# Kernel tuning notes

Measured on AMD Instinct MI355X. Metric: run time of the kernel, lower is better.

## Reference

```python
import jax, jax.numpy as jnp
import numpy as np

SR = 48000
TIME_LENGTH = 62400  # int(1.3 * 48000)
MAX_VOICES = 16


def _conv1d_same(x, k, b):
    # x: [B, L, Cin], k: [K, Cin, Cout] -> [B, L, Cout], keras Conv1D padding='same'
    y = jax.lax.conv_general_dilated(x, k, (1,), 'SAME', dimension_numbers=('NWC', 'WIO', 'NWC'))
    return y + b


def setup_inputs() -> dict:
    key = jax.random.key(0)
    ks = jax.random.split(key, 20)
    B, L, D, C = 16, 250, 128, 32
    V = MAX_VOICES
    din = D + C
    w = lambda k, s: jax.random.normal(k, s, jnp.float32) * 0.05
    inp = {}
    inp['base_signal'] = jax.random.normal(ks[0], (B, TIME_LENGTH), jnp.float32)
    inp['z'] = jax.random.normal(ks[1], (B, L, D), jnp.float32)
    inp['cond'] = jax.random.uniform(ks[2], (B, C), jnp.float32)
    inp['fundamental_freq'] = jax.random.uniform(ks[3], (B,), jnp.float32)
    # param_predictor: Dense(256)->Dense(128)->Dense(64)->Dense(4)
    inp['W1'] = w(ks[4], (din, 256)); inp['b1'] = jnp.zeros((256,), jnp.float32)
    inp['W2'] = w(ks[5], (256, 128)); inp['b2'] = jnp.zeros((128,), jnp.float32)
    inp['W3'] = w(ks[6], (128, 64));  inp['b3'] = jnp.zeros((64,), jnp.float32)
    inp['W4'] = w(ks[7], (64, 4));    inp['b4'] = jnp.zeros((4,), jnp.float32)
    # voice_gain_net: Conv1D(128,7)->Conv1D(64,5)->Conv1D(V,3), input channels = D + C
    inp['K1'] = w(ks[8], (7, din, 128)); inp['cb1'] = jnp.zeros((128,), jnp.float32)
    inp['K2'] = w(ks[9], (5, 128, 64));  inp['cb2'] = jnp.zeros((64,), jnp.float32)
    inp['K3'] = w(ks[10], (3, 64, V));   inp['cb3'] = jnp.zeros((V,), jnp.float32)
    return inp


def reference(base_signal, z, cond, fundamental_freq,
              W1, b1, W2, b2, W3, b3, W4, b4,
              K1, cb1, K2, cb2, K3, cb3):
    B, T = base_signal.shape
    L = z.shape[1]
    V = MAX_VOICES
    # ---- global param predictor ----
    z_global = jnp.mean(z, axis=1)
    x = jnp.concatenate([z_global, cond], axis=-1)
    h = jax.nn.relu(x @ W1 + b1)
    h = jax.nn.relu(h @ W2 + b2)
    h = jax.nn.relu(h @ W3 + b3)
    params = h @ W4 + b4  # [B,4]
    num_voices = 1.0 + 14.0 * jax.nn.sigmoid(params[:, 0:1])  # [B,1]
    detune_cents = params[:, 1:2] * 50.0                       # [B,1] (unused downstream, as in source)
    spread = jax.nn.sigmoid(params[:, 2:3])                    # [B,1]
    depth = jax.nn.sigmoid(params[:, 3:4]) * 0.5               # [B,1]
    # ---- per-voice gain envelopes at latent rate ----
    z_cond = jnp.concatenate([z, jnp.broadcast_to(cond[:, None, :], (B, L, cond.shape[-1]))], axis=-1)
    g = jax.nn.relu(_conv1d_same(z_cond, K1, cb1))
    g = jax.nn.relu(_conv1d_same(g, K2, cb2))
    g = _conv1d_same(g, K3, cb3)  # [B, L, V]
    # TF bilinear resize (half-pixel centers) L -> T along time axis
    scale = L / T
    src = jnp.clip((jnp.arange(T, dtype=jnp.float32) + 0.5) * scale - 0.5, 0.0, L - 1.0)
    i0 = jnp.floor(src).astype(jnp.int32)
    i1 = jnp.minimum(i0 + 1, L - 1)
    frac = (src - i0.astype(jnp.float32))[None, :, None]
    vg = g[:, i0, :] * (1.0 - frac) + g[:, i1, :] * frac
    voice_gains = jax.nn.softplus(vg)  # [B, T, V]
    # ---- 16-voice detune/roll/LFO-modulate/accumulate, vectorized over voices ----
    pos = (np.arange(V) - (V - 1) / 2.0) / V            # static [V]
    shifts = np.trunc(pos * 20.0).astype(np.int64)      # int() truncation as in source
    gidx = (np.arange(T)[None, :] - shifts[:, None]) % T  # static [V, T] gather for tf.roll
    shifted = base_signal[:, jnp.asarray(gidx)]         # [B, V, T]
    t = jnp.arange(T, dtype=jnp.float32) / SR
    lfo_freq = 3.0 + 0.3 * jnp.arange(V, dtype=jnp.float32)
    lfo = jnp.sin(2.0 * np.pi * lfo_freq[:, None] * t[None, :])  # [V, T]
    modulated = shifted * (1.0 + 0.2 * depth[:, 0][:, None, None] * lfo[None])  # [B, V, T]
    pan = 1.0 - jnp.abs(jnp.asarray(pos, dtype=jnp.float32))[None, :] * spread * 0.5  # [B, V]
    unison = jnp.einsum('bvt,btv,bv->bt', modulated, voice_gains, pan)  # [B, T]
    # ---- soft voice-count mask and normalization ----
    voice_mask = jax.nn.sigmoid((num_voices - jnp.arange(V, dtype=jnp.float32)[None, :]) * 2.0)  # [B, V]
    norm = jnp.sqrt(jnp.sum(voice_mask, axis=-1, keepdims=True) + 1e-6)  # [B, 1]
    gain_sum = jnp.einsum('btv,bv->bt', voice_gains, voice_mask)  # [B, T]
    return gain_sum / (norm + 1e-6) * unison
```

## Files before the change

### kernel.cpp

```cpp
#include <hip/hip_runtime.h>
#include <hip/hip_bf16.h>
#include <math.h>

#define L_LEN 250
#define D_DIM 128
#define C_DIM 32
#define DIN   160
#define NV    16
#define T_LEN 62400
#define CB    244
#define XROWS 272
#define NXB   (16 * XROWS * 160)
#define NK1   (128 * 1120)

typedef short short8 __attribute__((ext_vector_type(8)));
typedef float f32x4  __attribute__((ext_vector_type(4)));

__global__ __launch_bounds__(256) void prep_kernel(
        const float* __restrict__ z, const float* __restrict__ cond,
        const float* __restrict__ K1,
        __hip_bfloat16* __restrict__ Xb, __hip_bfloat16* __restrict__ K1t) {
    int idx = blockIdx.x * 256 + threadIdx.x;
    if (idx < NXB) {
        int b   = idx / (XROWS * 160);
        int rem = idx - b * (XROWS * 160);
        int r   = rem / 160;
        int ic  = rem - r * 160;
        int l   = r - 3;
        float v = 0.f;
        if (l >= 0 && l < L_LEN)
            v = (ic < D_DIM) ? z[((size_t)b * L_LEN + l) * D_DIM + ic]
                             : cond[b * C_DIM + (ic - D_DIM)];
        Xb[idx] = __float2bfloat16(v);
    } else if (idx < NXB + NK1) {
        int j  = idx - NXB;
        int oc = j / 1120;
        int k  = j - oc * 1120;
        K1t[j] = __float2bfloat16(K1[(size_t)k * 128 + oc]);
    }
}

__global__ __launch_bounds__(256) void conv1_mfma_mlp_kernel(
        const short* __restrict__ Xb, const short* __restrict__ K1t,
        float* __restrict__ g1,
        const float* __restrict__ z, const float* __restrict__ cond,
        const float* __restrict__ W1, const float* __restrict__ b1,
        const float* __restrict__ W2, const float* __restrict__ b2,
        const float* __restrict__ W3, const float* __restrict__ b3,
        const float* __restrict__ W4, const float* __restrict__ b4,
        float* __restrict__ P) {
    int tid = threadIdx.x;
    if (blockIdx.x < 16) {
        int b = blockIdx.x;
        __shared__ float buf[2176];
        float* xb = buf;
        float* h1 = buf + 160;
        float* h2 = buf + 416;
        float* h3 = buf + 544;
        float* pr = buf + 608;
        float* red = buf + 640;
        float4* sm4 = (float4*)(buf + 1152);
        {
            int c4 = tid & 31, rg = tid >> 5;
            const float4* zp = (const float4*)(z + (size_t)b * L_LEN * D_DIM) + c4;
            float4 acc = make_float4(0.f, 0.f, 0.f, 0.f);
            for (int r = rg; r < L_LEN; r += 8) {
                float4 v = zp[(size_t)r * 32];
                acc.x += v.x; acc.y += v.y; acc.z += v.z; acc.w += v.w;
            }
            sm4[rg * 32 + c4] = acc;
        }
        __syncthreads();
        if (tid < 32) {
            float4 acc = sm4[tid];
            #pragma unroll
            for (int g = 1; g < 8; ++g) {
                float4 v = sm4[g * 32 + tid];
                acc.x += v.x; acc.y += v.y; acc.z += v.z; acc.w += v.w;
            }
            const float inv = 1.0f / (float)L_LEN;
            acc.x *= inv; acc.y *= inv; acc.z *= inv; acc.w *= inv;
            ((float4*)xb)[tid] = acc;
        } else if (tid >= 128 && tid < DIN) {
            xb[tid] = cond[b * C_DIM + (tid - 128)];
        }
        __syncthreads();
        {
            const float* w = W1 + tid;
            float a0 = b1[tid], a1 = 0.f, a2 = 0.f, a3 = 0.f;
            #pragma unroll 4
            for (int i = 0; i < DIN; i += 4) {
                a0 = fmaf(xb[i],     w[(size_t)(i)     * 256], a0);
                a1 = fmaf(xb[i + 1], w[(size_t)(i + 1) * 256], a1);
                a2 = fmaf(xb[i + 2], w[(size_t)(i + 2) * 256], a2);
                a3 = fmaf(xb[i + 3], w[(size_t)(i + 3) * 256], a3);
            }
            h1[tid] = fmaxf((a0 + a1) + (a2 + a3), 0.f);
        }
        __syncthreads();
        {
            int oc = tid & 127, hh = tid >> 7;
            const float* w = W2 + (size_t)(hh * 128) * 128 + oc;
            const float* x = h1 + hh * 128;
            float a0 = 0.f, a1 = 0.f, a2 = 0.f, a3 = 0.f;
            #pragma unroll 4
            for (int i = 0; i < 128; i += 4) {
                a0 = fmaf(x[i],     w[(size_t)(i)     * 128], a0);
                a1 = fmaf(x[i + 1], w[(size_t)(i + 1) * 128], a1);
                a2 = fmaf(x[i + 2], w[(size_t)(i + 2) * 128], a2);
                a3 = fmaf(x[i + 3], w[(size_t)(i + 3) * 128], a3);
            }
            red[tid] = (a0 + a1) + (a2 + a3);
        }
        __syncthreads();
        if (tid < 128) h2[tid] = fmaxf(red[tid] + red[tid + 128] + b2[tid], 0.f);
        __syncthreads();
        {
            int oc = tid & 63, qg = tid >> 6;
            const float* w = W3 + (size_t)(qg * 32) * 64 + oc;
            const float* x = h2 + qg * 32;
            float a0 = 0.f, a1 = 0.f;
            #pragma unroll 4
            for (int i = 0; i < 32; i += 2) {
                a0 = fmaf(x[i],     w[(size_t)(i)     * 64], a0);
                a1 = fmaf(x[i + 1], w[(size_t)(i + 1) * 64], a1);
            }
            red[tid] = a0 + a1;
        }
        __syncthreads();
        if (tid < 64)
            h3[tid] = fmaxf(red[tid] + red[tid + 64] + red[tid + 128] + red[tid + 192] + b3[tid], 0.f);
        __syncthreads();
        red[tid] = h3[tid >> 2] * W4[(tid >> 2) * 4 + (tid & 3)];
        __syncthreads();
        if (tid < 4) {
            float s = b4[tid];
            for (int k = 0; k < 64; ++k) s += red[k * 4 + tid];
            pr[tid] = s;
        }
        __syncthreads();
        if (tid == 0) {
            float num_voices = 1.0f + 14.0f / (1.0f + __expf(-pr[0]));
            float spread     = 1.0f / (1.0f + __expf(-pr[2]));
            float depth      = 0.5f / (1.0f + __expf(-pr[3]));
            float* Pb = P + b * 40;
            float msum = 0.f;
            for (int v = 0; v < NV; ++v) {
                float m = 1.0f / (1.0f + __expf(-(num_voices - (float)v) * 2.0f));
                msum += m;
                Pb[2 + v] = m;
                float pos = ((float)v - 7.5f) * (1.0f / 16.0f);
                Pb[2 + NV + v] = 1.0f - fabsf(pos) * spread * 0.5f;
            }
            float norm = sqrtf(msum + 1e-6f);
            Pb[0] = depth;
            Pb[1] = 1.0f / (norm + 1e-6f);
        }
        return;
    }
    int blk = blockIdx.x - 16;
    int b   = blk >> 4;
    int lt  = blk & 15;
    int l0  = lt * 16;
    int lane = tid & 63;
    int oc0g = (tid >> 6) * 32;
    int m  = lane & 15;
    int kg = lane >> 4;

    const short* Ab = Xb + ((size_t)(b * XROWS + l0 + m) * 160 + kg * 8);
    const short* Bb = K1t + ((size_t)(oc0g + m) * 1120 + kg * 8);

    f32x4 acc0 = {0.f, 0.f, 0.f, 0.f};
    f32x4 acc1 = {0.f, 0.f, 0.f, 0.f};
    #pragma unroll 1
    for (int tap = 0; tap < 7; ++tap) {
        const short* ap = Ab + tap * 160;
        const short* bp = Bb + tap * 160;
        #pragma unroll
        for (int ks = 0; ks < 5; ++ks) {
            short8 av  = *(const short8*)(ap + ks * 32);
            short8 bv0 = *(const short8*)(bp + ks * 32);
            short8 bv1 = *(const short8*)(bp + 16 * 1120 + ks * 32);
            acc0 = __builtin_amdgcn_mfma_f32_16x16x32_bf16(av, bv0, acc0, 0, 0, 0);
            acc1 = __builtin_amdgcn_mfma_f32_16x16x32_bf16(av, bv1, acc1, 0, 0, 0);
        }
    }
    int rbase = l0 + kg * 4;
    #pragma unroll
    for (int j = 0; j < 4; ++j) {
        int lr = rbase + j;
        if (lr < L_LEN) {
            float* gp = g1 + ((size_t)b * L_LEN + lr) * 128 + oc0g + m;
            gp[0]  = acc0[j];
            gp[16] = acc1[j];
        }
    }
}

__global__ __launch_bounds__(256) void conv2_ws_kernel(
        const float* __restrict__ g1, const float* __restrict__ cb1,
        const float* __restrict__ K2, float* __restrict__ parts2) {
    int tid = threadIdx.x;
    __shared__ float kw[16 * 5 * 64];
    __shared__ float smr[16][72];
    int s  = blockIdx.x >> 6;
    int b  = (blockIdx.x >> 2) & 15;
    int lt = blockIdx.x & 3;
    int l0 = lt * 62;

    for (int idx = tid; idx < 16 * 5 * 64; idx += 256) {
        int oc = idx & 63;
        int r  = idx >> 6;
        int tap = r % 5, ic = r / 5;
        kw[idx] = K2[((size_t)tap * 128 + s * 16 + ic) * 64 + oc];
    }
    for (int idx = tid; idx < 68 * 16; idx += 256) {
        int ch = idx & 15;
        int pl = idx >> 4;
        int p  = l0 - 2 + pl;
        int gi = s * 16 + ch;
        float v = 0.f;
        if (p >= 0 && p < L_LEN)
            v = fmaxf(g1[((size_t)b * L_LEN + p) * 128 + gi] + cb1[gi], 0.f);
        smr[ch][pl] = v;
    }
    __syncthreads();

    int oc0 = (tid & 31) << 1;
    int lb  = (tid >> 5) << 3;
    float acc[2][8];
    #pragma unroll
    for (int j = 0; j < 8; ++j) { acc[0][j] = 0.f; acc[1][j] = 0.f; }

    #pragma unroll 2
    for (int ic = 0; ic < 16; ++ic) {
        float zr[12];
        *(float4*)&zr[0] = *(const float4*)&smr[ic][lb];
        *(float4*)&zr[4] = *(const float4*)&smr[ic][lb + 4];
        *(float4*)&zr[8] = *(const float4*)&smr[ic][lb + 8];
        const float* kwp = &kw[ic * 5 * 64 + oc0];
        #pragma unroll
        for (int tap = 0; tap < 5; ++tap) {
            float2 w = *(const float2*)(kwp + tap * 64);
            #pragma unroll
            for (int j = 0; j < 8; ++j) {
                acc[0][j] = fmaf(zr[tap + j], w.x, acc[0][j]);
                acc[1][j] = fmaf(zr[tap + j], w.y, acc[1][j]);
            }
        }
    }
    float* po = parts2 + (size_t)s * (16 * L_LEN * 64)
              + (size_t)b * L_LEN * 64 + oc0;
    #pragma unroll
    for (int j = 0; j < 8; ++j) {
        int l = l0 + lb + j;
        if (l < L_LEN)
            *(float2*)(po + (size_t)l * 64) = make_float2(acc[0][j], acc[1][j]);
    }
}

__global__ __launch_bounds__(256) void conv3_main_kernel(
        const float* __restrict__ base, const float* __restrict__ parts2,
        const float* __restrict__ cb2,
        const float* __restrict__ K3, const float* __restrict__ cb3,
        const float* __restrict__ P, float* __restrict__ out) {
    int b = blockIdx.x / CB;
    int c = blockIdx.x % CB;
    int t0 = c * 256;
    int tid = threadIdx.x;
    const int PSTR2 = 16 * L_LEN * 64;
    const float scale = 250.0f / 62400.0f;

    __shared__ float k3t[16][196];
    __shared__ float sA[6][68];
    __shared__ float g3loc[4][17];
    __shared__ float Pb[34];

    float src0 = ((float)t0 + 0.5f) * scale - 0.5f;
    src0 = fminf(fmaxf(src0, 0.0f), 249.0f);
    int L0 = (int)floorf(src0);

    if (tid < 34) Pb[tid] = P[b * 40 + tid];
    for (int idx = tid; idx < 3 * 64 * 16; idx += 256) {
        int v  = idx & 15;
        int ti = idx >> 4;
        k3t[v][ti] = K3[ti * 16 + v];
    }
    for (int idx = tid; idx < 6 * 64; idx += 256) {
        int pl = idx >> 6;
        int i  = idx & 63;
        int p  = L0 - 1 + pl;
        float v = 0.f;
        if (p >= 0 && p < L_LEN) {
            size_t o = ((size_t)b * L_LEN + p) * 64 + i;
            float a = cb2[i];
            #pragma unroll
            for (int k = 0; k < 8; ++k) a += parts2[o + (size_t)k * PSTR2];
            v = fmaxf(a, 0.f);
        }
        sA[pl][i] = v;
    }
    __syncthreads();

    {
        int seg = tid & 3;
        int v   = (tid >> 2) & 15;
        int r   = tid >> 6;
        float acc = 0.f;
        #pragma unroll
        for (int tap = 0; tap < 3; ++tap) {
            const float* gr = &sA[r + tap][seg * 16];
            const float* kr = &k3t[v][tap * 64 + seg * 16];
            #pragma unroll
            for (int j = 0; j < 4; ++j) {
                float4 g = *(const float4*)&gr[j * 4];
                float4 k = *(const float4*)&kr[j * 4];
                acc = fmaf(g.x, k.x, acc);
                acc = fmaf(g.y, k.y, acc);
                acc = fmaf(g.z, k.z, acc);
                acc = fmaf(g.w, k.w, acc);
            }
        }
        acc += __shfl_xor(acc, 1);
        acc += __shfl_xor(acc, 2);
        if (seg == 0) g3loc[r][v] = acc + cb3[v];
    }
    __syncthreads();

    int t = t0 + tid;
    if (t >= T_LEN) return;
    float depth = Pb[0];
    float coef  = Pb[1];
    float src = ((float)t + 0.5f) * scale - 0.5f;
    src = fminf(fmaxf(src, 0.0f), 249.0f);
    float fi0 = floorf(src);
    int i0 = (int)fi0;
    int i1 = min(i0 + 1, L_LEN - 1);
    float frac = src - fi0;
    int r0 = i0 - L0;
    int r1 = i1 - L0;
    float vg[16];
    #pragma unroll
    for (int v = 0; v < NV; ++v) {
        float a = g3loc[r0][v];
        float d = g3loc[r1][v];
        vg[v] = fmaf(d - a, frac, a);
    }
    float tsec = (float)t * (1.0f / 48000.0f);
    const float* bs = base + (size_t)b * T_LEN;
    const int shifts[NV] = {-9,-8,-6,-5,-4,-3,-1,0,0,1,3,4,5,6,8,9};
    float gain_sum = 0.f, uni = 0.f;
    #pragma unroll
    for (int v = 0; v < NV; ++v) {
        float x = vg[v];
        float sp = fmaxf(x, 0.f) + __logf(1.0f + __expf(-fabsf(x)));
        float fv = 3.0f + 0.3f * (float)v;
        float ph = fv * tsec;
        ph -= floorf(ph);
        float lfo = __builtin_amdgcn_sinf(ph);
        int tb = t - shifts[v];
        if (tb < 0) tb += T_LEN; else if (tb >= T_LEN) tb -= T_LEN;
        float mod = bs[tb] * fmaf(0.2f * depth, lfo, 1.0f);
        gain_sum = fmaf(sp, Pb[2 + v], gain_sum);
        uni      = fmaf(mod * sp, Pb[2 + NV + v], uni);
    }
    out[(size_t)b * T_LEN + t] = gain_sum * coef * uni;
}

__global__ void params_kernel(const float* __restrict__ z, const float* __restrict__ cond,
                              const float* __restrict__ W1, const float* __restrict__ b1,
                              const float* __restrict__ W2, const float* __restrict__ b2,
                              const float* __restrict__ W3, const float* __restrict__ b3,
                              const float* __restrict__ W4, const float* __restrict__ b4,
                              float* __restrict__ P) {
    int b = blockIdx.x;
    int tid = threadIdx.x;
    __shared__ float xb[DIN];
    __shared__ float zp2[128];
    __shared__ float h1[256];
    __shared__ float h2[128];
    __shared__ float h3[64];
    __shared__ float pr[4];
    {
        int i = tid & 127, half = tid >> 7;
        const float* zp = z + (size_t)b * L_LEN * D_DIM + i;
        float s = 0.f;
        for (int l = half; l < L_LEN; l += 2) s += zp[(size_t)l * D_DIM];
        if (half) zp2[i] = s;
        __syncthreads();
        if (!half) xb[i] = (s + zp2[i]) * (1.0f / (float)L_LEN);
        if (tid >= 128 && tid < DIN) xb[tid] = cond[b * C_DIM + (tid - 128)];
    }
    __syncthreads();
    {
        float acc = b1[tid];
        for (int i = 0; i < DIN; ++i) acc = fmaf(xb[i], W1[i * 256 + tid], acc);
        h1[tid] = fmaxf(acc, 0.f);
    }
    __syncthreads();
    if (tid < 128) {
        float acc = b2[tid];
        for (int i = 0; i < 256; ++i) acc = fmaf(h1[i], W2[i * 128 + tid], acc);
        h2[tid] = fmaxf(acc, 0.f);
    }
    __syncthreads();
    if (tid < 64) {
        float acc = b3[tid];
        for (int i = 0; i < 128; ++i) acc = fmaf(h2[i], W3[i * 64 + tid], acc);
        h3[tid] = fmaxf(acc, 0.f);
    }
    __syncthreads();
    if (tid < 4) {
        float acc = b4[tid];
        for (int i = 0; i < 64; ++i) acc = fmaf(h3[i], W4[i * 4 + tid], acc);
        pr[tid] = acc;
    }
    __syncthreads();
    if (tid == 0) {
        float num_voices = 1.0f + 14.0f / (1.0f + __expf(-pr[0]));
        float spread     = 1.0f / (1.0f + __expf(-pr[2]));
        float depth      = 0.5f / (1.0f + __expf(-pr[3]));
        float* Pb = P + b * 40;
        float msum = 0.f;
        for (int v = 0; v < NV; ++v) {
            float m = 1.0f / (1.0f + __expf(-(num_voices - (float)v) * 2.0f));
            msum += m;
            Pb[2 + v] = m;
            float pos = ((float)v - 7.5f) * (1.0f / 16.0f);
            Pb[2 + NV + v] = 1.0f - fabsf(pos) * spread * 0.5f;
        }
        float norm = sqrtf(msum + 1e-6f);
        Pb[0] = depth;
        Pb[1] = 1.0f / (norm + 1e-6f);
    }
}

__global__ void conv1_mono_kernel(const float* __restrict__ z, const float* __restrict__ cond,
                                  const float* __restrict__ K1, const float* __restrict__ cb1,
                                  float* __restrict__ g1) {
    int b  = blockIdx.x >> 4;
    int lt = blockIdx.x & 15;
    int l0 = lt * 16;
    int tid = threadIdx.x;
    __shared__ float sm[DIN][22];
    for (int idx = tid; idx < 22 * DIN; idx += 256) {
        int pl = idx / DIN;
        int i  = idx - pl * DIN;
        int p  = l0 - 3 + pl;
        float v = 0.f;
        if (p >= 0 && p < L_LEN)
            v = (i < D_DIM) ? z[((size_t)b * L_LEN + p) * D_DIM + i]
                            : cond[b * C_DIM + (i - D_DIM)];
        sm[i][pl] = v;
    }
    __syncthreads();
    int oc = tid & 127;
    int lb = (tid >> 7) * 8;
    float bias = cb1[oc];
    float acc[8];
    #pragma unroll
    for (int j = 0; j < 8; ++j) acc[j] = bias;
    for (int i = 0; i < DIN; ++i) {
        float zr[14];
        #pragma unroll
        for (int q = 0; q < 14; ++q) zr[q] = sm[i][lb + q];
        #pragma unroll
        for (int tap = 0; tap < 7; ++tap) {
            float k = K1[(size_t)(tap * DIN + i) * 128 + oc];
            #pragma unroll
            for (int j = 0; j < 8; ++j) acc[j] = fmaf(zr[tap + j], k, acc[j]);
        }
    }
    #pragma unroll
    for (int j = 0; j < 8; ++j) {
        int l = l0 + lb + j;
        if (l < L_LEN) g1[((size_t)b * L_LEN + l) * 128 + oc] = fmaxf(acc[j], 0.f);
    }
}

__global__ void conv2_mono_kernel(const float* __restrict__ g1,
                                  const float* __restrict__ K2, const float* __restrict__ cb2,
                                  float* __restrict__ g2) {
    int b  = blockIdx.x >> 4;
    int lt = blockIdx.x & 15;
    int l0 = lt * 16;
    int tid = threadIdx.x;
    __shared__ float sm[128][20];
    for (int idx = tid; idx < 20 * 128; idx += 256) {
        int pl = idx >> 7;
        int i  = idx & 127;
        int p  = l0 - 2 + pl;
        float v = (p >= 0 && p < L_LEN) ? g1[((size_t)b * L_LEN + p) * 128 + i] : 0.f;
        sm[i][pl] = v;
    }
    __syncthreads();
    int oc = tid & 63;
    int lb = (tid >> 6) * 4;
    float bias = cb2[oc];
    float acc[4];
    #pragma unroll
    for (int j = 0; j < 4; ++j) acc[j] = bias;
    for (int i = 0; i < 128; ++i) {
        float zr[8];
        #pragma unroll
        for (int q = 0; q < 8; ++q) zr[q] = sm[i][lb + q];
        #pragma unroll
        for (int tap = 0; tap < 5; ++tap) {
            float k = K2[(size_t)(tap * 128 + i) * 64 + oc];
            #pragma unroll
            for (int j = 0; j < 4; ++j) acc[j] = fmaf(zr[tap + j], k, acc[j]);
        }
    }
    #pragma unroll
    for (int j = 0; j < 4; ++j) {
        int l = l0 + lb + j;
        if (l < L_LEN) g2[((size_t)b * L_LEN + l) * 64 + oc] = fmaxf(acc[j], 0.f);
    }
}

__global__ void conv3_mono_kernel(const float* __restrict__ g2,
                                  const float* __restrict__ K3, const float* __restrict__ cb3,
                                  float* __restrict__ g3) {
    int b  = blockIdx.x >> 4;
    int lt = blockIdx.x & 15;
    int l0 = lt * 16;
    int tid = threadIdx.x;
    int v  = tid & 15;
    int ll = tid >> 4;
    int l  = l0 + ll;
    if (l >= L_LEN) return;
    float acc = cb3[v];
    #pragma unroll
    for (int tap = 0; tap < 3; ++tap) {
        int p = l + tap - 1;
        if (p < 0 || p >= L_LEN) continue;
        const float* gp = g2 + ((size_t)b * L_LEN + p) * 64;
        #pragma unroll
        for (int i = 0; i < 64; ++i) acc = fmaf(gp[i], K3[(size_t)(tap * 64 + i) * 16 + v], acc);
    }
    g3[((size_t)b * L_LEN + l) * 16 + v] = acc;
}

__global__ __launch_bounds__(256) void main_mono_kernel(
        const float* __restrict__ base, const float* __restrict__ g3,
        const float* __restrict__ P, float* __restrict__ out) {
    int b = blockIdx.x / CB;
    int c = blockIdx.x % CB;
    int t = c * 256 + threadIdx.x;
    __shared__ float Pb[34];
    if (threadIdx.x < 34) Pb[threadIdx.x] = P[b * 40 + threadIdx.x];
    __syncthreads();
    if (t >= T_LEN) return;
    float depth = Pb[0];
    float coef  = Pb[1];
    const float scale = 250.0f / 62400.0f;
    float src = ((float)t + 0.5f) * scale - 0.5f;
    src = fminf(fmaxf(src, 0.0f), 249.0f);
    float fi0 = floorf(src);
    int i0 = (int)fi0;
    int i1 = min(i0 + 1, L_LEN - 1);
    float frac = src - fi0;
    const float4* r0 = (const float4*)(g3 + ((size_t)b * L_LEN + i0) * NV);
    const float4* r1 = (const float4*)(g3 + ((size_t)b * L_LEN + i1) * NV);
    float vg[16];
    #pragma unroll
    for (int q = 0; q < 4; ++q) {
        float4 a = r0[q];
        float4 d = r1[q];
        vg[q * 4 + 0] = fmaf(d.x - a.x, frac, a.x);
        vg[q * 4 + 1] = fmaf(d.y - a.y, frac, a.y);
        vg[q * 4 + 2] = fmaf(d.z - a.z, frac, a.z);
        vg[q * 4 + 3] = fmaf(d.w - a.w, frac, a.w);
    }
    float tsec = (float)t * (1.0f / 48000.0f);
    const float* bs = base + (size_t)b * T_LEN;
    const int shifts[NV] = {-9,-8,-6,-5,-4,-3,-1,0,0,1,3,4,5,6,8,9};
    float gain_sum = 0.f, uni = 0.f;
    #pragma unroll
    for (int v = 0; v < NV; ++v) {
        float x = vg[v];
        float sp = fmaxf(x, 0.f) + __logf(1.0f + __expf(-fabsf(x)));
        float fv = 3.0f + 0.3f * (float)v;
        float ph = fv * tsec;
        ph -= floorf(ph);
        float lfo = __builtin_amdgcn_sinf(ph);
        int tb = t - shifts[v];
        if (tb < 0) tb += T_LEN; else if (tb >= T_LEN) tb -= T_LEN;
        float mod = bs[tb] * fmaf(0.2f * depth, lfo, 1.0f);
        gain_sum = fmaf(sp, Pb[2 + v], gain_sum);
        uni      = fmaf(mod * sp, Pb[2 + NV + v], uni);
    }
    out[(size_t)b * T_LEN + t] = gain_sum * coef * uni;
}

extern "C" void kernel_launch(void* const* d_in, const int* in_sizes, int n_in,
                              void* d_out, int out_size, void* d_ws, size_t ws_size,
                              hipStream_t stream) {
    const float* base = (const float*)d_in[0];
    const float* z    = (const float*)d_in[1];
    const float* cond = (const float*)d_in[2];
    const float* W1 = (const float*)d_in[4];  const float* b1 = (const float*)d_in[5];
    const float* W2 = (const float*)d_in[6];  const float* b2 = (const float*)d_in[7];
    const float* W3 = (const float*)d_in[8];  const float* b3 = (const float*)d_in[9];
    const float* W4 = (const float*)d_in[10]; const float* b4 = (const float*)d_in[11];
    const float* K1 = (const float*)d_in[12]; const float* cb1 = (const float*)d_in[13];
    const float* K2 = (const float*)d_in[14]; const float* cb2 = (const float*)d_in[15];
    const float* K3 = (const float*)d_in[16]; const float* cb3 = (const float*)d_in[17];
    float* out = (float*)d_out;

    int B = in_sizes[0] / T_LEN;

    float* ws = (float*)d_ws;
    const size_t XBF = NXB / 2;
    const size_t K1F = NK1 / 2;
    const size_t G1  = (size_t)16 * L_LEN * 128;
    const size_t P2  = (size_t)16 * L_LEN * 64;
    size_t need = (1024 + XBF + K1F + G1 + 8 * P2) * sizeof(float);

    float* P = ws;
    if (ws_size >= need) {
        __hip_bfloat16* Xb  = (__hip_bfloat16*)(ws + 1024);
        __hip_bfloat16* K1t = (__hip_bfloat16*)(ws + 1024 + XBF);
        float* g1     = ws + 1024 + XBF + K1F;
        float* parts2 = g1 + G1;

        int prep_blocks = (NXB + NK1 + 255) / 256;
        prep_kernel<<<prep_blocks, 256, 0, stream>>>(z, cond, K1, Xb, K1t);
        conv1_mfma_mlp_kernel<<<16 + 256, 256, 0, stream>>>(
            (const short*)Xb, (const short*)K1t, g1, z, cond,
            W1, b1, W2, b2, W3, b3, W4, b4, P);
        conv2_ws_kernel<<<512, 256, 0, stream>>>(g1, cb1, K2, parts2);
        conv3_main_kernel<<<B * CB, 256, 0, stream>>>(base, parts2, cb2, K3, cb3, P, out);
    } else {
        float* g1 = ws + 1024;
        float* g2 = g1 + (size_t)B * L_LEN * 128;
        float* g3 = g2 + (size_t)B * L_LEN * 64;
        params_kernel<<<B, 256, 0, stream>>>(z, cond, W1, b1, W2, b2, W3, b3, W4, b4, P);
        conv1_mono_kernel<<<B * 16, 256, 0, stream>>>(z, cond, K1, cb1, g1);
        conv2_mono_kernel<<<B * 16, 256, 0, stream>>>(g1, K2, cb2, g2);
        conv3_mono_kernel<<<B * 16, 256, 0, stream>>>(g2, K3, cb3, g3);
        main_mono_kernel<<<B * CB, 256, 0, stream>>>(base, g3, P, out);
    }
}
```

Before: 68.76 us.

## Move conv2 to bf16 MFMA with fused bias/ReLU and padded bf16 activations

Replaces the fp32 split-K conv2 kernel, which wrote eight partial sums, with a bf16 MFMA kernel. It reads a zero-padded bf16 copy of conv1 output that conv1 now writes with bias and ReLU already applied. conv3 then reads a single g2 buffer instead of summing eight partials. This removes the partial-sum traffic and the scalar FMA work, at the cost of bf16 rounding on the conv2 inputs and weights and extra prep work to transpose K2 and zero the pad rows.

```diff
diff --git a/kernel.cpp b/kernel.cpp
--- a/kernel.cpp
+++ b/kernel.cpp
@@ -10,16 +10,20 @@
 #define T_LEN 62400
 #define CB    244
 #define XROWS 272
+#define XR2   256
 #define NXB   (16 * XROWS * 160)
 #define NK1   (128 * 1120)
+#define NK2   (64 * 640)
+#define NPAD  (16 * 6 * 128)
 
 typedef short short8 __attribute__((ext_vector_type(8)));
 typedef float f32x4  __attribute__((ext_vector_type(4)));
 
 __global__ __launch_bounds__(256) void prep_kernel(
         const float* __restrict__ z, const float* __restrict__ cond,
-        const float* __restrict__ K1,
-        __hip_bfloat16* __restrict__ Xb, __hip_bfloat16* __restrict__ K1t) {
+        const float* __restrict__ K1, const float* __restrict__ K2,
+        __hip_bfloat16* __restrict__ Xb, __hip_bfloat16* __restrict__ K1t,
+        __hip_bfloat16* __restrict__ K2t, __hip_bfloat16* __restrict__ g1b) {
     int idx = blockIdx.x * 256 + threadIdx.x;
     if (idx < NXB) {
         int b   = idx / (XROWS * 160);
@@ -37,12 +41,25 @@
         int oc = j / 1120;
         int k  = j - oc * 1120;
         K1t[j] = __float2bfloat16(K1[(size_t)k * 128 + oc]);
+    } else if (idx < NXB + NK1 + NK2) {
+        int j  = idx - NXB - NK1;
+        int oc = j / 640;
+        int k  = j - oc * 640;
+        K2t[j] = __float2bfloat16(K2[(size_t)k * 64 + oc]);
+    } else if (idx < NXB + NK1 + NK2 + NPAD) {
+        int j  = idx - NXB - NK1 - NK2;
+        int b  = j / (6 * 128);
+        int rem = j - b * (6 * 128);
+        int rr = rem >> 7;
+        int ic = rem & 127;
+        int r  = (rr < 2) ? rr : 250 + rr;
+        g1b[((size_t)b * XR2 + r) * 128 + ic] = __float2bfloat16(0.f);
     }
 }
 
 __global__ __launch_bounds__(256) void conv1_mfma_mlp_kernel(
         const short* __restrict__ Xb, const short* __restrict__ K1t,
-        float* __restrict__ g1,
+        const float* __restrict__ cb1, __hip_bfloat16* __restrict__ g1b,
         const float* __restrict__ z, const float* __restrict__ cond,
         const float* __restrict__ W1, const float* __restrict__ b1,
         const float* __restrict__ W2, const float* __restrict__ b2,
@@ -185,82 +202,58 @@
             acc1 = __builtin_amdgcn_mfma_f32_16x16x32_bf16(av, bv1, acc1, 0, 0, 0);
         }
     }
+    float bias0 = cb1[oc0g + m];
+    float bias1 = cb1[oc0g + m + 16];
     int rbase = l0 + kg * 4;
     #pragma unroll
     for (int j = 0; j < 4; ++j) {
         int lr = rbase + j;
         if (lr < L_LEN) {
-            float* gp = g1 + ((size_t)b * L_LEN + lr) * 128 + oc0g + m;
-            gp[0]  = acc0[j];
-            gp[16] = acc1[j];
-        }
-    }
-}
-
-__global__ __launch_bounds__(256) void conv2_ws_kernel(
-        const float* __restrict__ g1, const float* __restrict__ cb1,
-        const float* __restrict__ K2, float* __restrict__ parts2) {
+            __hip_bfloat16* gp = g1b + ((size_t)(b * XR2) + lr + 2) * 128 + oc0g + m;
+            gp[0]  = __float2bfloat16(fmaxf(acc0[j] + bias0, 0.f));
+            gp[16] = __float2bfloat16(fmaxf(acc1[j] + bias1, 0.f));
+        }
+    }
+}
+
+__global__ __launch_bounds__(256) void conv2_mfma_kernel(
+        const short* __restrict__ g1b, const short* __restrict__ K2t,
+        float* __restrict__ g2) {
     int tid = threadIdx.x;
-    __shared__ float kw[16 * 5 * 64];
-    __shared__ float smr[16][72];
-    int s  = blockIdx.x >> 6;
-    int b  = (blockIdx.x >> 2) & 15;
-    int lt = blockIdx.x & 3;
-    int l0 = lt * 62;
-
-    for (int idx = tid; idx < 16 * 5 * 64; idx += 256) {
-        int oc = idx & 63;
-        int r  = idx >> 6;
-        int tap = r % 5, ic = r / 5;
-        kw[idx] = K2[((size_t)tap * 128 + s * 16 + ic) * 64 + oc];
-    }
-    for (int idx = tid; idx < 68 * 16; idx += 256) {
-        int ch = idx & 15;
-        int pl = idx >> 4;
-        int p  = l0 - 2 + pl;
-        int gi = s * 16 + ch;
-        float v = 0.f;
-        if (p >= 0 && p < L_LEN)
-            v = fmaxf(g1[((size_t)b * L_LEN + p) * 128 + gi] + cb1[gi], 0.f);
-        smr[ch][pl] = v;
-    }
-    __syncthreads();
-
-    int oc0 = (tid & 31) << 1;
-    int lb  = (tid >> 5) << 3;
-    float acc[2][8];
-    #pragma unroll
-    for (int j = 0; j < 8; ++j) { acc[0][j] = 0.f; acc[1][j] = 0.f; }
-
-    #pragma unroll 2
-    for (int ic = 0; ic < 16; ++ic) {
-        float zr[12];
-        *(float4*)&zr[0] = *(const float4*)&smr[ic][lb];
-        *(float4*)&zr[4] = *(const float4*)&smr[ic][lb + 4];
-        *(float4*)&zr[8] = *(const float4*)&smr[ic][lb + 8];
-        const float* kwp = &kw[ic * 5 * 64 + oc0];
-        #pragma unroll
-        for (int tap = 0; tap < 5; ++tap) {
-            float2 w = *(const float2*)(kwp + tap * 64);
-            #pragma unroll
-            for (int j = 0; j < 8; ++j) {
-                acc[0][j] = fmaf(zr[tap + j], w.x, acc[0][j]);
-                acc[1][j] = fmaf(zr[tap + j], w.y, acc[1][j]);
-            }
-        }
-    }
-    float* po = parts2 + (size_t)s * (16 * L_LEN * 64)
-              + (size_t)b * L_LEN * 64 + oc0;
-    #pragma unroll
-    for (int j = 0; j < 8; ++j) {
-        int l = l0 + lb + j;
+    int b   = blockIdx.x >> 4;
+    int lt  = blockIdx.x & 15;
+    int l0  = lt * 16;
+    int lane = tid & 63;
+    int oc0w = (tid >> 6) * 16;
+    int m  = lane & 15;
+    int kg = lane >> 4;
+
+    const short* Ab = g1b + ((size_t)(b * XR2 + l0 + m) * 128 + kg * 8);
+    const short* Bb = K2t + ((size_t)(oc0w + m) * 640 + kg * 8);
+
+    f32x4 acc = {0.f, 0.f, 0.f, 0.f};
+    #pragma unroll 1
+    for (int tap = 0; tap < 5; ++tap) {
+        const short* ap = Ab + tap * 128;
+        const short* bp = Bb + tap * 128;
+        #pragma unroll
+        for (int ks = 0; ks < 4; ++ks) {
+            short8 av = *(const short8*)(ap + ks * 32);
+            short8 bv = *(const short8*)(bp + ks * 32);
+            acc = __builtin_amdgcn_mfma_f32_16x16x32_bf16(av, bv, acc, 0, 0, 0);
+        }
+    }
+    int rbase = l0 + kg * 4;
+    #pragma unroll
+    for (int j = 0; j < 4; ++j) {
+        int l = rbase + j;
         if (l < L_LEN)
-            *(float2*)(po + (size_t)l * 64) = make_float2(acc[0][j], acc[1][j]);
+            g2[((size_t)b * L_LEN + l) * 64 + oc0w + m] = acc[j];
     }
 }
 
 __global__ __launch_bounds__(256) void conv3_main_kernel(
-        const float* __restrict__ base, const float* __restrict__ parts2,
+        const float* __restrict__ base, const float* __restrict__ g2,
         const float* __restrict__ cb2,
         const float* __restrict__ K3, const float* __restrict__ cb3,
         const float* __restrict__ P, float* __restrict__ out) {
@@ -268,7 +261,6 @@
     int c = blockIdx.x % CB;
     int t0 = c * 256;
     int tid = threadIdx.x;
-    const int PSTR2 = 16 * L_LEN * 64;
     const float scale = 250.0f / 62400.0f;
 
     __shared__ float k3t[16][196];
@@ -291,13 +283,8 @@
         int i  = idx & 63;
         int p  = L0 - 1 + pl;
         float v = 0.f;
-        if (p >= 0 && p < L_LEN) {
-            size_t o = ((size_t)b * L_LEN + p) * 64 + i;
-            float a = cb2[i];
-            #pragma unroll
-            for (int k = 0; k < 8; ++k) a += parts2[o + (size_t)k * PSTR2];
-            v = fmaxf(a, 0.f);
-        }
+        if (p >= 0 && p < L_LEN)
+            v = fmaxf(cb2[i] + g2[((size_t)b * L_LEN + p) * 64 + i], 0.f);
         sA[pl][i] = v;
     }
     __syncthreads();
@@ -611,26 +598,29 @@
     int B = in_sizes[0] / T_LEN;
 
     float* ws = (float*)d_ws;
-    const size_t XBF = NXB / 2;
-    const size_t K1F = NK1 / 2;
-    const size_t G1  = (size_t)16 * L_LEN * 128;
-    const size_t P2  = (size_t)16 * L_LEN * 64;
-    size_t need = (1024 + XBF + K1F + G1 + 8 * P2) * sizeof(float);
+    const size_t XBF  = NXB / 2;
+    const size_t K1F  = NK1 / 2;
+    const size_t K2F  = NK2 / 2;
+    const size_t G1BF = (size_t)16 * XR2 * 128 / 2;
+    const size_t G2   = (size_t)16 * L_LEN * 64;
+    size_t need = (1024 + XBF + K1F + K2F + G1BF + G2) * sizeof(float);
 
     float* P = ws;
     if (ws_size >= need) {
         __hip_bfloat16* Xb  = (__hip_bfloat16*)(ws + 1024);
         __hip_bfloat16* K1t = (__hip_bfloat16*)(ws + 1024 + XBF);
-        float* g1     = ws + 1024 + XBF + K1F;
-        float* parts2 = g1 + G1;
-
-        int prep_blocks = (NXB + NK1 + 255) / 256;
-        prep_kernel<<<prep_blocks, 256, 0, stream>>>(z, cond, K1, Xb, K1t);
+        __hip_bfloat16* K2t = (__hip_bfloat16*)(ws + 1024 + XBF + K1F);
+        __hip_bfloat16* g1b = (__hip_bfloat16*)(ws + 1024 + XBF + K1F + K2F);
+        float* g2 = ws + 1024 + XBF + K1F + K2F + G1BF;
+
+        int prep_blocks = (NXB + NK1 + NK2 + NPAD + 255) / 256;
+        prep_kernel<<<prep_blocks, 256, 0, stream>>>(z, cond, K1, K2, Xb, K1t, K2t, g1b);
         conv1_mfma_mlp_kernel<<<16 + 256, 256, 0, stream>>>(
-            (const short*)Xb, (const short*)K1t, g1, z, cond,
+            (const short*)Xb, (const short*)K1t, cb1, g1b, z, cond,
             W1, b1, W2, b2, W3, b3, W4, b4, P);
-        conv2_ws_kernel<<<512, 256, 0, stream>>>(g1, cb1, K2, parts2);
-        conv3_main_kernel<<<B * CB, 256, 0, stream>>>(base, parts2, cb2, K3, cb3, P, out);
+        conv2_mfma_kernel<<<256, 256, 0, stream>>>(
+            (const short*)g1b, (const short*)K2t, g2);
+        conv3_main_kernel<<<B * CB, 256, 0, stream>>>(base, g2, cb2, K3, cb3, P, out);
     } else {
         float* g1 = ws + 1024;
         float* g2 = g1 + (size_t)B * L_LEN * 128;
```

After: 58.87 us. 1.17x faster.
